# Performance work log

Measured on AMD Instinct MI355X. Metric: run time of the kernel, lower is better.

The kernel has to match this reference:

```python
import jax, jax.numpy as jnp
import numpy as np

DIM = 1024
HID = 512
N_EXPERTS = 16
TOP_K = 4


def setup_inputs() -> dict:
    key = jax.random.key(0)
    ks = jax.random.split(key, 8)
    s = 0.02
    x = jax.random.normal(ks[0], (2, 1024, DIM), dtype=jnp.float32)
    gate_w = jax.random.normal(ks[1], (N_EXPERTS, DIM), dtype=jnp.float32) * s
    # stacked expert weights (nn.Linear stores [out, in]; we keep [E, out, in])
    w1 = jax.random.normal(ks[2], (N_EXPERTS, HID, DIM), dtype=jnp.float32) * s
    w3 = jax.random.normal(ks[3], (N_EXPERTS, HID, DIM), dtype=jnp.float32) * s
    w2 = jax.random.normal(ks[4], (N_EXPERTS, DIM, HID), dtype=jnp.float32) * s
    sw1 = jax.random.normal(ks[5], (HID, DIM), dtype=jnp.float32) * s
    sw3 = jax.random.normal(ks[6], (HID, DIM), dtype=jnp.float32) * s
    sw2 = jax.random.normal(ks[7], (DIM, HID), dtype=jnp.float32) * s
    return {"x": x, "gate_w": gate_w, "w1": w1, "w3": w3, "w2": w2,
            "sw1": sw1, "sw3": sw3, "sw2": sw2}


def reference(x, gate_w, w1, w3, w2, sw1, sw3, sw2):
    bsz, seq_len, dim = x.shape
    xf = x.reshape(-1, dim)                              # [T, d]
    T = xf.shape[0]

    # router: softmax -> top-k -> renormalize
    probs = jax.nn.softmax(xf @ gate_w.T, axis=-1)       # [T, E]
    top_w, top_idx = jax.lax.top_k(probs, TOP_K)         # [T, K]
    top_w = top_w / jnp.sum(top_w, axis=-1, keepdims=True)

    # combine weights as dense [T, E] (zero for unselected experts);
    # weighted dense per-expert compute is mathematically identical to the
    # gather/scatter loop since unselected experts get weight 0.
    rows = jnp.arange(T)[:, None]
    combine = jnp.zeros((T, N_EXPERTS), dtype=xf.dtype).at[rows, top_idx].set(top_w)

    h1 = jnp.einsum('td,ehd->teh', xf, w1)               # [T, E, h]
    h3 = jnp.einsum('td,ehd->teh', xf, w3)
    act = jax.nn.silu(h1) * h3
    eout = jnp.einsum('teh,edh->ted', act, w2)           # [T, E, d]
    moe_out = jnp.einsum('ted,te->td', eout, combine)    # [T, d]

    shared = (jax.nn.silu(xf @ sw1.T) * (xf @ sw3.T)) @ sw2.T
    return (moe_out + shared).reshape(bsz, seq_len, dim)
```

## Files before the change

### kernel.cpp

```cpp
#include <hip/hip_runtime.h>

#define DIM   1024
#define HID   512
#define NEXP  16
#define TOPK  4
#define SLOTS 5
#define PITCH 72
#define MAXT128 96

typedef unsigned short u16;
typedef unsigned int   u32;
typedef short bf16x8 __attribute__((ext_vector_type(8)));
typedef float f32x4  __attribute__((ext_vector_type(4)));

__device__ __forceinline__ float bf2f(u16 u) {
    union { u32 i; float f; } v; v.i = ((u32)u) << 16; return v.f;
}
__device__ __forceinline__ u16 f2bf(float f) {
    union { float f; u32 i; } v; v.f = f;
    u32 lsb = (v.i >> 16) & 1u;
    v.i += 0x7fffu + lsb;
    return (u16)(v.i >> 16);
}
__device__ __forceinline__ uint4 pack8(float4 a, float4 b) {
    uint4 r;
    r.x = (u32)f2bf(a.x) | ((u32)f2bf(a.y) << 16);
    r.y = (u32)f2bf(a.z) | ((u32)f2bf(a.w) << 16);
    r.z = (u32)f2bf(b.x) | ((u32)f2bf(b.y) << 16);
    r.w = (u32)f2bf(b.z) | ((u32)f2bf(b.w) << 16);
    return r;
}

#define CW ((size_t)NEXP * HID * DIM / 8)
#define CS ((size_t)HID * DIM / 8)
#define SEG_B0 (CW)
#define SEG_B1 (SEG_B0 + CS)
#define SEG_B2 (SEG_B1 + CW)
#define SEG_B3 (SEG_B2 + CS)
#define SEG_B4 (SEG_B3 + CW)
#define SEG_B5 (SEG_B4 + CS)

__global__ __launch_bounds__(256) void moe_prep(
    const float* __restrict__ x,    const float* __restrict__ gate,
    const float* __restrict__ w1,   const float* __restrict__ w3,
    const float* __restrict__ w2,   const float* __restrict__ sw1,
    const float* __restrict__ sw3,  const float* __restrict__ sw2,
    u16* __restrict__ dst, int nCvt,
    int* __restrict__ counts, u32* __restrict__ pairs,
    float* __restrict__ wslot, int T)
{
    const int blk = blockIdx.x;
    if (blk < nCvt) {
        const size_t c = (size_t)blk * 256 + threadIdx.x;
        const float* src; size_t loc;
        if      (c < SEG_B0) { src = w1;  loc = c; }
        else if (c < SEG_B1) { src = sw1; loc = c - SEG_B0; }
        else if (c < SEG_B2) { src = w3;  loc = c - SEG_B1; }
        else if (c < SEG_B3) { src = sw3; loc = c - SEG_B2; }
        else if (c < SEG_B4) { src = w2;  loc = c - SEG_B3; }
        else if (c < SEG_B5) { src = sw2; loc = c - SEG_B4; }
        else                 { src = x;   loc = c - SEG_B5; }
        float4 a = ((const float4*)src)[loc * 2];
        float4 b = ((const float4*)src)[loc * 2 + 1];
        ((uint4*)dst)[c] = pack8(a, b);
        return;
    }
    const int lane = threadIdx.x;
    if (lane >= 64) return;
    const int t = blk - nCvt;
    const float* xrow = x + (size_t)t * DIM;
    float xr[16];
#pragma unroll
    for (int j = 0; j < 16; ++j) xr[j] = xrow[lane + 64 * j];

    float logit[NEXP];
#pragma unroll
    for (int e = 0; e < NEXP; ++e) {
        const float* g = gate + (size_t)e * DIM;
        float s = 0.f;
#pragma unroll
        for (int j = 0; j < 16; ++j) s += xr[j] * g[lane + 64 * j];
#pragma unroll
        for (int off = 32; off > 0; off >>= 1) s += __shfl_xor(s, off);
        logit[e] = s;
    }
    float v[NEXP];
#pragma unroll
    for (int e = 0; e < NEXP; ++e) v[e] = logit[e];
    int idx[TOPK]; float lv[TOPK];
#pragma unroll
    for (int r = 0; r < TOPK; ++r) {
        int be = 0; float bv = v[0];
        for (int e = 1; e < NEXP; ++e) { if (v[e] > bv) { bv = v[e]; be = e; } }
        idx[r] = be; lv[r] = bv; v[be] = -3.0e38f;
    }
    float wk[TOPK]; float wsum = 0.f;
#pragma unroll
    for (int r = 0; r < TOPK; ++r) { wk[r] = __expf(lv[r] - lv[0]); wsum += wk[r]; }
#pragma unroll
    for (int r = 0; r < TOPK; ++r) wk[r] /= wsum;

    if (lane < TOPK) {
        int e = idx[lane];
        int slot = atomicAdd(&counts[e], 1);
        if (slot < T) pairs[(size_t)e * T + slot] = ((u32)t << 3) | (u32)lane;
        wslot[t * SLOTS + lane] = wk[lane];
    } else if (lane == TOPK) {
        pairs[(size_t)NEXP * T + t] = ((u32)t << 3) | 4u;
        wslot[t * SLOTS + 4] = 1.0f;
    }
}

__global__ __launch_bounds__(64) void moe_build_tiles(
    const int* __restrict__ counts,
    int* __restrict__ tileE, int* __restrict__ tileR0, int* __restrict__ tileNV,
    int* __restrict__ tot, int T)
{
    const int lane = threadIdx.x;
    int c = 0;
    if (lane < NEXP)       c = min(max(counts[lane], 0), T);
    else if (lane == NEXP) c = T;
    int nt = (c + 127) >> 7;
    int pre = nt;
    for (int off = 1; off < 32; off <<= 1) {
        int vv = __shfl_up(pre, off);
        if (lane >= off) pre += vv;
    }
    int excl = pre - nt;
    if (lane <= NEXP) {
        for (int i = 0; i < nt; ++i) {
            int id = excl + i;
            if (id < MAXT128) {
                tileE[id] = lane; tileR0[id] = i << 7;
                tileNV[id] = min(128, c - (i << 7));
            }
        }
        if (lane == NEXP) *tot = min(excl + nt, MAXT128);
    }
}

__global__ __launch_bounds__(256) void moe_gemm1(
    const u16* __restrict__ xb,
    const u16* __restrict__ w1c, const u16* __restrict__ w3c,
    const u32* __restrict__ pairs,
    const int* __restrict__ tileE, const int* __restrict__ tileR0,
    const int* __restrict__ tileNV, const int* __restrict__ tot,
    u16* __restrict__ act, int T)
{
    const int tile = blockIdx.y;
    if (tile >= min(*tot, MAXT128)) return;
    const int e  = min(max(tileE[tile], 0), NEXP);
    const int r0 = min(max(tileR0[tile], 0), T - 1);
    const int nv = min(max(tileNV[tile], 0), min(128, T - r0));
    const int n0 = blockIdx.x * 64;

    const u16* W1 = w1c + (size_t)e * HID * DIM;
    const u16* W3 = w3c + (size_t)e * HID * DIM;

    __shared__ __align__(16) u16 sA [128 * PITCH];
    __shared__ __align__(16) u16 sB1[ 64 * PITCH];
    __shared__ __align__(16) u16 sB3[ 64 * PITCH];
    __shared__ u32 sEnt[128];

    const int tid = threadIdx.x;
    if (tid < 128) {
        u32 ent = (tid < nv) ? pairs[(size_t)e * T + r0 + tid] : 0u;
        u32 tk = ent >> 3, sl = ent & 7u;
        if (tk >= (u32)T) tk = 0;
        if (sl >= SLOTS)  sl = 0;
        sEnt[tid] = (tk << 3) | sl;
    }
    __syncthreads();

    const int ar = tid >> 1;
    const int ac = (tid & 1) * 32;
    const u16* xrow = xb + (size_t)(sEnt[ar] >> 3) * DIM;
    const int br = tid >> 2;
    const int bc = (tid & 3) * 16;
    const u16* b1row = W1 + (size_t)(n0 + br) * DIM;
    const u16* b3row = W3 + (size_t)(n0 + br) * DIM;

    const int wv   = tid >> 6;
    const int lane = tid & 63;
    const int l15  = lane & 15;
    const int kq   = (lane >> 4) * 8;
    const int m0   = wv * 32;

    f32x4 acc1[2][4], acc3[2][4];
#pragma unroll
    for (int i = 0; i < 2; ++i)
#pragma unroll
        for (int j = 0; j < 4; ++j) { acc1[i][j] = (f32x4){0,0,0,0}; acc3[i][j] = (f32x4){0,0,0,0}; }

    for (int kt = 0; kt < DIM; kt += 64) {
        __syncthreads();
        *(uint4*)&sA [ar*PITCH + ac]      = *(const uint4*)&xrow [kt + ac];
        *(uint4*)&sA [ar*PITCH + ac +  8] = *(const uint4*)&xrow [kt + ac +  8];
        *(uint4*)&sA [ar*PITCH + ac + 16] = *(const uint4*)&xrow [kt + ac + 16];
        *(uint4*)&sA [ar*PITCH + ac + 24] = *(const uint4*)&xrow [kt + ac + 24];
        *(uint4*)&sB1[br*PITCH + bc]      = *(const uint4*)&b1row[kt + bc];
        *(uint4*)&sB1[br*PITCH + bc +  8] = *(const uint4*)&b1row[kt + bc + 8];
        *(uint4*)&sB3[br*PITCH + bc]      = *(const uint4*)&b3row[kt + bc];
        *(uint4*)&sB3[br*PITCH + bc +  8] = *(const uint4*)&b3row[kt + bc + 8];
        __syncthreads();
#pragma unroll
        for (int ks = 0; ks < 64; ks += 32) {
            bf16x8 a0 = *(const bf16x8*)&sA[(m0      + l15)*PITCH + ks + kq];
            bf16x8 a1 = *(const bf16x8*)&sA[(m0 + 16 + l15)*PITCH + ks + kq];
#pragma unroll
            for (int nt = 0; nt < 4; ++nt) {
                bf16x8 b1 = *(const bf16x8*)&sB1[(nt*16 + l15)*PITCH + ks + kq];
                bf16x8 b3 = *(const bf16x8*)&sB3[(nt*16 + l15)*PITCH + ks + kq];
                acc1[0][nt] = __builtin_amdgcn_mfma_f32_16x16x32_bf16(a0, b1, acc1[0][nt], 0, 0, 0);
                acc1[1][nt] = __builtin_amdgcn_mfma_f32_16x16x32_bf16(a1, b1, acc1[1][nt], 0, 0, 0);
                acc3[0][nt] = __builtin_amdgcn_mfma_f32_16x16x32_bf16(a0, b3, acc3[0][nt], 0, 0, 0);
                acc3[1][nt] = __builtin_amdgcn_mfma_f32_16x16x32_bf16(a1, b3, acc3[1][nt], 0, 0, 0);
            }
        }
    }
#pragma unroll
    for (int mf = 0; mf < 2; ++mf)
#pragma unroll
    for (int nt = 0; nt < 4; ++nt)
#pragma unroll
    for (int r = 0; r < 4; ++r) {
        int ml = m0 + mf*16 + (lane >> 4)*4 + r;
        if (ml < nv) {
            float h1 = acc1[mf][nt][r], h3 = acc3[mf][nt][r];
            float a = (h1 / (1.f + __expf(-h1))) * h3;
            u32 ent = sEnt[ml];
            size_t sidx = (size_t)(ent >> 3) * SLOTS + (ent & 7u);
            act[sidx * HID + n0 + nt*16 + l15] = f2bf(a);
        }
    }
}

__global__ __launch_bounds__(256) void moe_gemm2(
    const u16* __restrict__ act, const u16* __restrict__ w2c,
    const u32* __restrict__ pairs, const float* __restrict__ wslot,
    const int* __restrict__ tileE, const int* __restrict__ tileR0,
    const int* __restrict__ tileNV, const int* __restrict__ tot,
    u16* __restrict__ eout, float* __restrict__ out, int useEout, int T)
{
    const int tile = blockIdx.y;
    if (tile >= min(*tot, MAXT128)) return;
    const int e  = min(max(tileE[tile], 0), NEXP);
    const int r0 = min(max(tileR0[tile], 0), T - 1);
    const int nv = min(max(tileNV[tile], 0), min(128, T - r0));
    const int n0 = blockIdx.x * 128;

    const u16* W2 = w2c + (size_t)e * DIM * HID;

    __shared__ __align__(16) u16 sA[128 * PITCH];
    __shared__ __align__(16) u16 sB[128 * PITCH];
    __shared__ u32 sEnt[128];

    const int tid = threadIdx.x;
    if (tid < 128) {
        u32 ent = (tid < nv) ? pairs[(size_t)e * T + r0 + tid] : 0u;
        u32 tk = ent >> 3, sl = ent & 7u;
        if (tk >= (u32)T) tk = 0;
        if (sl >= SLOTS)  sl = 0;
        sEnt[tid] = (tk << 3) | sl;
    }
    __syncthreads();

    const int ar = tid >> 1;
    const int ac = (tid & 1) * 32;
    const u32 entA = sEnt[ar];
    const u16* arow = act + ((size_t)(entA >> 3) * SLOTS + (entA & 7u)) * HID;
    const u16* brow = W2 + (size_t)(n0 + ar) * HID;

    const int wv   = tid >> 6;
    const int lane = tid & 63;
    const int l15  = lane & 15;
    const int kq   = (lane >> 4) * 8;
    const int m0   = (wv & 1) * 64;
    const int nc0  = (wv >> 1) * 64;

    f32x4 acc[4][4];
#pragma unroll
    for (int i = 0; i < 4; ++i)
#pragma unroll
        for (int j = 0; j < 4; ++j) acc[i][j] = (f32x4){0,0,0,0};

    for (int kt = 0; kt < HID; kt += 64) {
        __syncthreads();
        *(uint4*)&sA[ar*PITCH + ac]      = *(const uint4*)&arow[kt + ac];
        *(uint4*)&sA[ar*PITCH + ac +  8] = *(const uint4*)&arow[kt + ac +  8];
        *(uint4*)&sA[ar*PITCH + ac + 16] = *(const uint4*)&arow[kt + ac + 16];
        *(uint4*)&sA[ar*PITCH + ac + 24] = *(const uint4*)&arow[kt + ac + 24];
        *(uint4*)&sB[ar*PITCH + ac]      = *(const uint4*)&brow[kt + ac];
        *(uint4*)&sB[ar*PITCH + ac +  8] = *(const uint4*)&brow[kt + ac +  8];
        *(uint4*)&sB[ar*PITCH + ac + 16] = *(const uint4*)&brow[kt + ac + 16];
        *(uint4*)&sB[ar*PITCH + ac + 24] = *(const uint4*)&brow[kt + ac + 24];
        __syncthreads();
#pragma unroll
        for (int ks = 0; ks < 64; ks += 32) {
            bf16x8 af[4], bf[4];
#pragma unroll
            for (int mf = 0; mf < 4; ++mf)
                af[mf] = *(const bf16x8*)&sA[(m0 + mf*16 + l15)*PITCH + ks + kq];
#pragma unroll
            for (int nf = 0; nf < 4; ++nf)
                bf[nf] = *(const bf16x8*)&sB[(nc0 + nf*16 + l15)*PITCH + ks + kq];
#pragma unroll
            for (int mf = 0; mf < 4; ++mf)
#pragma unroll
                for (int nf = 0; nf < 4; ++nf)
                    acc[mf][nf] = __builtin_amdgcn_mfma_f32_16x16x32_bf16(af[mf], bf[nf], acc[mf][nf], 0, 0, 0);
        }
    }
#pragma unroll
    for (int mf = 0; mf < 4; ++mf)
#pragma unroll
    for (int nf = 0; nf < 4; ++nf)
#pragma unroll
    for (int r = 0; r < 4; ++r) {
        int ml = m0 + mf*16 + (lane >> 4)*4 + r;
        if (ml < nv) {
            u32 ent = sEnt[ml];
            u32 tk = ent >> 3;
            float cw = wslot[tk * SLOTS + (ent & 7u)];
            int col = n0 + nc0 + nf*16 + l15;
            float v = cw * acc[mf][nf][r];
            if (useEout) {
                size_t sidx = (size_t)tk * SLOTS + (ent & 7u);
                eout[sidx * DIM + col] = f2bf(v);
            } else {
                atomicAdd(&out[(size_t)tk * DIM + col], v);
            }
        }
    }
}

__global__ __launch_bounds__(256) void moe_combine(
    const u16* __restrict__ eout, float* __restrict__ out, int n4)
{
    int i = blockIdx.x * 256 + threadIdx.x;
    if (i >= n4) return;
    int o4 = i * 4;
    int t = o4 >> 10;
    int col = o4 & 1023;
    float a0 = 0.f, a1 = 0.f, a2 = 0.f, a3 = 0.f;
#pragma unroll
    for (int s = 0; s < SLOTS; ++s) {
        const u16* row = eout + ((size_t)t * SLOTS + s) * DIM + col;
        ushort4 u = *(const ushort4*)row;
        a0 += bf2f(u.x); a1 += bf2f(u.y); a2 += bf2f(u.z); a3 += bf2f(u.w);
    }
    float4* op = (float4*)(out + (size_t)t * DIM + col);
    *op = (float4){a0, a1, a2, a3};
}

extern "C" void kernel_launch(void* const* d_in, const int* in_sizes, int n_in,
                              void* d_out, int out_size, void* d_ws, size_t ws_size,
                              hipStream_t stream)
{
    (void)n_in; (void)out_size;
    const float* x    = (const float*)d_in[0];
    const float* gate = (const float*)d_in[1];
    const float* w1   = (const float*)d_in[2];
    const float* w3   = (const float*)d_in[3];
    const float* w2   = (const float*)d_in[4];
    const float* sw1  = (const float*)d_in[5];
    const float* sw3  = (const float*)d_in[6];
    const float* sw2  = (const float*)d_in[7];
    float* out = (float*)d_out;
    const int T = in_sizes[0] / DIM;

    char* w = (char*)d_ws;
    int*  counts = (int*)(w);
    int*  tileE  = (int*)(w + 256);
    int*  tileR0 = (int*)(w + 256 + 512);
    int*  tileNV = (int*)(w + 256 + 1024);
    int*  tot    = (int*)(w + 256 + 1536);
    size_t off = 4096;
    u32*   pairs = (u32*)(w + off);  off += (size_t)(NEXP + 1) * T * 4;
    float* wslot = (float*)(w + off); off += (size_t)T * SLOTS * 4;
    off = (off + 255) & ~(size_t)255;
    u16*   actb  = (u16*)(w + off);  off += (size_t)T * SLOTS * HID * 2;
    off = (off + 255) & ~(size_t)255;
    u16*   cvtb  = (u16*)(w + off);
    const size_t xChunks = (size_t)T * DIM / 8;
    const size_t cvtChunks = SEG_B5 + xChunks;
    off += cvtChunks * 8 * 2;
    off = (off + 255) & ~(size_t)255;
    u16*   eoutb = (u16*)(w + off);
    const size_t needEout = off + (size_t)T * SLOTS * DIM * 2;

    u16* W1c = cvtb;
    u16* W3c = cvtb + SEG_B1 * 8;
    u16* W2c = cvtb + SEG_B3 * 8;
    u16* xb  = cvtb + SEG_B5 * 8;

    const int useEout = (ws_size >= needEout) ? 1 : 0;

    hipMemsetAsync(w, 0, 256, stream);
    if (!useEout)
        hipMemsetAsync(out, 0, (size_t)T * DIM * sizeof(float), stream);

    const int nCvt = (int)(cvtChunks / 256);
    moe_prep<<<nCvt + T, 256, 0, stream>>>(
        x, gate, w1, w3, w2, sw1, sw3, sw2, cvtb, nCvt, counts, pairs, wslot, T);
    moe_build_tiles<<<1, 64, 0, stream>>>(counts, tileE, tileR0, tileNV, tot, T);

    moe_gemm1<<<dim3(HID / 64, MAXT128), 256, 0, stream>>>(
        xb, W1c, W3c, pairs, tileE, tileR0, tileNV, tot, actb, T);
    moe_gemm2<<<dim3(DIM / 128, MAXT128), 256, 0, stream>>>(
        actb, W2c, pairs, wslot, tileE, tileR0, tileNV, tot, eoutb, out, useEout, T);
    if (useEout)
        moe_combine<<<(T * DIM / 4 + 255) / 256, 256, 0, stream>>>(
            eoutb, out, T * DIM / 4);
}
```

Before: 261.3 us.

## Drop tile-build kernel, index GEMM tiles directly by expert and row block

Removes the moe_build_tiles launch. The GEMM kernels now derive expert and row offset straight from blockIdx.y over a fixed grid of 17x16 tiles and exit early when a block lies past that expert's count. The prep kernel also puts router blocks first, spreads the 16 gate dot products across 4 waves through shared memory, and converts two chunks per thread in the weight-conversion blocks. This saves one launch and its serialisation point, but launches many more empty GEMM blocks and hard-caps each expert at 16 tiles of 128 rows, which only holds when T is at most 2048.

Result: slower. 266.9 us (+2.1%).

```diff
diff --git a/kernel.cpp b/kernel.cpp
--- a/kernel.cpp
+++ b/kernel.cpp
@@ -6,7 +6,7 @@
 #define TOPK  4
 #define SLOTS 5
 #define PITCH 72
-#define MAXT128 96
+#define TPE   16
 
 typedef unsigned short u16;
 typedef unsigned int   u32;
@@ -45,48 +45,59 @@
     const float* __restrict__ w1,   const float* __restrict__ w3,
     const float* __restrict__ w2,   const float* __restrict__ sw1,
     const float* __restrict__ sw3,  const float* __restrict__ sw2,
-    u16* __restrict__ dst, int nCvt,
+    u16* __restrict__ dst,
     int* __restrict__ counts, u32* __restrict__ pairs,
     float* __restrict__ wslot, int T)
 {
     const int blk = blockIdx.x;
-    if (blk < nCvt) {
-        const size_t c = (size_t)blk * 256 + threadIdx.x;
-        const float* src; size_t loc;
-        if      (c < SEG_B0) { src = w1;  loc = c; }
-        else if (c < SEG_B1) { src = sw1; loc = c - SEG_B0; }
-        else if (c < SEG_B2) { src = w3;  loc = c - SEG_B1; }
-        else if (c < SEG_B3) { src = sw3; loc = c - SEG_B2; }
-        else if (c < SEG_B4) { src = w2;  loc = c - SEG_B3; }
-        else if (c < SEG_B5) { src = sw2; loc = c - SEG_B4; }
-        else                 { src = x;   loc = c - SEG_B5; }
-        float4 a = ((const float4*)src)[loc * 2];
-        float4 b = ((const float4*)src)[loc * 2 + 1];
-        ((uint4*)dst)[c] = pack8(a, b);
+    const int tid = threadIdx.x;
+    if (blk >= T) {
+        const size_t base = (size_t)(blk - T) * 512 + tid;
+        const size_t totC = SEG_B5 + ((size_t)T << 7);
+#pragma unroll
+        for (int h = 0; h < 2; ++h) {
+            const size_t c = base + (size_t)h * 256;
+            if (c >= totC) break;
+            const float* src; size_t loc;
+            if      (c < SEG_B0) { src = w1;  loc = c; }
+            else if (c < SEG_B1) { src = sw1; loc = c - SEG_B0; }
+            else if (c < SEG_B2) { src = w3;  loc = c - SEG_B1; }
+            else if (c < SEG_B3) { src = sw3; loc = c - SEG_B2; }
+            else if (c < SEG_B4) { src = w2;  loc = c - SEG_B3; }
+            else if (c < SEG_B5) { src = sw2; loc = c - SEG_B4; }
+            else                 { src = x;   loc = c - SEG_B5; }
+            float4 a = ((const float4*)src)[loc * 2];
+            float4 b = ((const float4*)src)[loc * 2 + 1];
+            ((uint4*)dst)[c] = pack8(a, b);
+        }
         return;
     }
-    const int lane = threadIdx.x;
-    if (lane >= 64) return;
-    const int t = blk - nCvt;
+    const int t    = blk;
+    const int lane = tid & 63;
+    const int wv   = tid >> 6;
     const float* xrow = x + (size_t)t * DIM;
     float xr[16];
 #pragma unroll
     for (int j = 0; j < 16; ++j) xr[j] = xrow[lane + 64 * j];
 
-    float logit[NEXP];
-#pragma unroll
-    for (int e = 0; e < NEXP; ++e) {
+    __shared__ float slog[NEXP];
+#pragma unroll
+    for (int i = 0; i < 4; ++i) {
+        const int e = wv * 4 + i;
         const float* g = gate + (size_t)e * DIM;
         float s = 0.f;
 #pragma unroll
         for (int j = 0; j < 16; ++j) s += xr[j] * g[lane + 64 * j];
 #pragma unroll
         for (int off = 32; off > 0; off >>= 1) s += __shfl_xor(s, off);
-        logit[e] = s;
-    }
+        if (lane == 0) slog[e] = s;
+    }
+    __syncthreads();
+    if (wv != 0) return;
+
     float v[NEXP];
 #pragma unroll
-    for (int e = 0; e < NEXP; ++e) v[e] = logit[e];
+    for (int e = 0; e < NEXP; ++e) v[e] = slog[e];
     int idx[TOPK]; float lv[TOPK];
 #pragma unroll
     for (int r = 0; r < TOPK; ++r) {
@@ -111,47 +122,17 @@
     }
 }
 
-__global__ __launch_bounds__(64) void moe_build_tiles(
-    const int* __restrict__ counts,
-    int* __restrict__ tileE, int* __restrict__ tileR0, int* __restrict__ tileNV,
-    int* __restrict__ tot, int T)
-{
-    const int lane = threadIdx.x;
-    int c = 0;
-    if (lane < NEXP)       c = min(max(counts[lane], 0), T);
-    else if (lane == NEXP) c = T;
-    int nt = (c + 127) >> 7;
-    int pre = nt;
-    for (int off = 1; off < 32; off <<= 1) {
-        int vv = __shfl_up(pre, off);
-        if (lane >= off) pre += vv;
-    }
-    int excl = pre - nt;
-    if (lane <= NEXP) {
-        for (int i = 0; i < nt; ++i) {
-            int id = excl + i;
-            if (id < MAXT128) {
-                tileE[id] = lane; tileR0[id] = i << 7;
-                tileNV[id] = min(128, c - (i << 7));
-            }
-        }
-        if (lane == NEXP) *tot = min(excl + nt, MAXT128);
-    }
-}
-
 __global__ __launch_bounds__(256) void moe_gemm1(
     const u16* __restrict__ xb,
     const u16* __restrict__ w1c, const u16* __restrict__ w3c,
-    const u32* __restrict__ pairs,
-    const int* __restrict__ tileE, const int* __restrict__ tileR0,
-    const int* __restrict__ tileNV, const int* __restrict__ tot,
+    const u32* __restrict__ pairs, const int* __restrict__ counts,
     u16* __restrict__ act, int T)
 {
-    const int tile = blockIdx.y;
-    if (tile >= min(*tot, MAXT128)) return;
-    const int e  = min(max(tileE[tile], 0), NEXP);
-    const int r0 = min(max(tileR0[tile], 0), T - 1);
-    const int nv = min(max(tileNV[tile], 0), min(128, T - r0));
+    const int e   = blockIdx.y >> 4;
+    const int r0  = (blockIdx.y & (TPE - 1)) << 7;
+    const int cnt = (e == NEXP) ? T : min(max(counts[e], 0), T);
+    if (r0 >= cnt) return;
+    const int nv = min(128, cnt - r0);
     const int n0 = blockIdx.x * 64;
 
     const u16* W1 = w1c + (size_t)e * HID * DIM;
@@ -238,15 +219,14 @@
 __global__ __launch_bounds__(256) void moe_gemm2(
     const u16* __restrict__ act, const u16* __restrict__ w2c,
     const u32* __restrict__ pairs, const float* __restrict__ wslot,
-    const int* __restrict__ tileE, const int* __restrict__ tileR0,
-    const int* __restrict__ tileNV, const int* __restrict__ tot,
+    const int* __restrict__ counts,
     u16* __restrict__ eout, float* __restrict__ out, int useEout, int T)
 {
-    const int tile = blockIdx.y;
-    if (tile >= min(*tot, MAXT128)) return;
-    const int e  = min(max(tileE[tile], 0), NEXP);
-    const int r0 = min(max(tileR0[tile], 0), T - 1);
-    const int nv = min(max(tileNV[tile], 0), min(128, T - r0));
+    const int e   = blockIdx.y >> 4;
+    const int r0  = (blockIdx.y & (TPE - 1)) << 7;
+    const int cnt = (e == NEXP) ? T : min(max(counts[e], 0), T);
+    if (r0 >= cnt) return;
+    const int nv = min(128, cnt - r0);
     const int n0 = blockIdx.x * 128;
 
     const u16* W2 = w2c + (size_t)e * DIM * HID;
@@ -371,10 +351,6 @@
 
     char* w = (char*)d_ws;
     int*  counts = (int*)(w);
-    int*  tileE  = (int*)(w + 256);
-    int*  tileR0 = (int*)(w + 256 + 512);
-    int*  tileNV = (int*)(w + 256 + 1024);
-    int*  tot    = (int*)(w + 256 + 1536);
     size_t off = 4096;
     u32*   pairs = (u32*)(w + off);  off += (size_t)(NEXP + 1) * T * 4;
     float* wslot = (float*)(w + off); off += (size_t)T * SLOTS * 4;
@@ -400,15 +376,14 @@
     if (!useEout)
         hipMemsetAsync(out, 0, (size_t)T * DIM * sizeof(float), stream);
 
-    const int nCvt = (int)(cvtChunks / 256);
-    moe_prep<<<nCvt + T, 256, 0, stream>>>(
-        x, gate, w1, w3, w2, sw1, sw3, sw2, cvtb, nCvt, counts, pairs, wslot, T);
-    moe_build_tiles<<<1, 64, 0, stream>>>(counts, tileE, tileR0, tileNV, tot, T);
-
-    moe_gemm1<<<dim3(HID / 64, MAXT128), 256, 0, stream>>>(
-        xb, W1c, W3c, pairs, tileE, tileR0, tileNV, tot, actb, T);
-    moe_gemm2<<<dim3(DIM / 128, MAXT128), 256, 0, stream>>>(
-        actb, W2c, pairs, wslot, tileE, tileR0, tileNV, tot, eoutb, out, useEout, T);
+    const int nCvt = (int)((cvtChunks + 511) / 512);
+    moe_prep<<<T + nCvt, 256, 0, stream>>>(
+        x, gate, w1, w3, w2, sw1, sw3, sw2, cvtb, counts, pairs, wslot, T);
+
+    moe_gemm1<<<dim3(HID / 64, (NEXP + 1) * TPE), 256, 0, stream>>>(
+        xb, W1c, W3c, pairs, counts, actb, T);
+    moe_gemm2<<<dim3(DIM / 128, (NEXP + 1) * TPE), 256, 0, stream>>>(
+        actb, W2c, pairs, wslot, counts, eoutb, out, useEout, T);
     if (useEout)
         moe_combine<<<(T * DIM / 4 + 255) / 256, 256, 0, stream>>>(
             eoutb, out, T * DIM / 4);
```
